# Optimization experiments

Hardware: AMD Instinct MI355X
Metric: run time of the kernel (lower is better)

The kernel has to match this reference:

```python
import jax, jax.numpy as jnp
import numpy as np

NEG_SLOPE = 0.2  # PyG GATv2Conv default negative_slope
HEADS = 4


def _gatv2_layer(x, src, dst, Wl, bl, Wr, br, att, bias):
    """GATv2Conv, concat=False (mean over heads), add_self_loops handled by caller.
    x: [N, Fin]; src/dst: [E] (message src -> dst); Wl/Wr: [Fin, H*C]; att: [H, C].
    """
    N = x.shape[0]
    H, C = att.shape
    xl = (x @ Wl + bl).reshape(N, H, C)  # source-side transform
    xr = (x @ Wr + br).reshape(N, H, C)  # target-side transform
    e = jax.nn.leaky_relu(xl[src] + xr[dst], NEG_SLOPE)          # [E, H, C]
    logits = jnp.einsum('ehc,hc->eh', e, att)                     # [E, H]
    # segment softmax over incoming edges of each target node
    m = jax.ops.segment_max(logits, dst, num_segments=N)          # [N, H]
    a = jnp.exp(logits - m[dst])
    denom = jax.ops.segment_sum(a, dst, num_segments=N)
    alpha = a / denom[dst]                                        # [E, H]
    out = jax.ops.segment_sum(alpha[:, :, None] * xl[src], dst, num_segments=N)  # [N, H, C]
    return out.mean(axis=1) + bias                                # concat=False -> head mean


def _glorot(k, shape):
    fan_in, fan_out = shape[0], shape[1] if len(shape) > 1 else shape[0]
    s = jnp.sqrt(2.0 / (fan_in + fan_out)).astype(jnp.float32)
    return jax.random.normal(k, shape, jnp.float32) * s


def setup_inputs() -> dict:
    key = jax.random.key(0)
    ks = jax.random.split(key, 24)
    N, E = 50000, 512000
    x = jax.random.normal(ks[0], (N, 9), jnp.float32)
    src = jax.random.randint(ks[1], (E,), 0, N, dtype=jnp.int32)
    dst = jax.random.randint(ks[2], (E,), 0, N, dtype=jnp.int32)
    dst = jnp.where(src == dst, (dst + 1) % N, dst)  # PyG removes self-loops then re-adds them
    edge_index = jnp.stack([src, dst])
    dims = [(9, 64), (64, 64), (64, 128)]  # (Fin, C_out) per layer
    inp = {'x': x, 'edge_index': edge_index}
    ki = 3
    for i, (fi, co) in enumerate(dims):
        inp[f'Wl{i}'] = _glorot(ks[ki], (fi, HEADS * co)); ki += 1
        inp[f'bl{i}'] = jnp.zeros((HEADS * co,), jnp.float32)
        inp[f'Wr{i}'] = _glorot(ks[ki], (fi, HEADS * co)); ki += 1
        inp[f'br{i}'] = jnp.zeros((HEADS * co,), jnp.float32)
        inp[f'att{i}'] = _glorot(ks[ki], (HEADS, co)); ki += 1
        inp[f'b{i}'] = jnp.zeros((co,), jnp.float32)
    return inp


def reference(x, edge_index, Wl0, bl0, Wr0, br0, att0, b0,
              Wl1, bl1, Wr1, br1, att1, b1,
              Wl2, bl2, Wr2, br2, att2, b2):
    N = x.shape[0]
    loops = jnp.arange(N, dtype=edge_index.dtype)
    src = jnp.concatenate([edge_index[0], loops])  # add self-loops (PyG default)
    dst = jnp.concatenate([edge_index[1], loops])
    h = _gatv2_layer(x, src, dst, Wl0, bl0, Wr0, br0, att0, b0)
    h = jax.nn.relu(h)  # dropout: eval mode -> identity
    h = _gatv2_layer(h, src, dst, Wl1, bl1, Wr1, br1, att1, b1)
    h = jax.nn.relu(h)
    out = _gatv2_layer(h, src, dst, Wl2, bl2, Wr2, br2, att2, b2)
    return out
```

## Files before the change

kernel.cpp:

```cpp
#include <hip/hip_runtime.h>
#include <hip/hip_bf16.h>


typedef __attribute__((ext_vector_type(8))) short bf16x8;
typedef __attribute__((ext_vector_type(4))) float f32x4;

__device__ __forceinline__ float bflo(unsigned w) { return __uint_as_float(w << 16); }
__device__ __forceinline__ float bfhi(unsigned w) { return __uint_as_float(w & 0xffff0000u); }
__device__ __forceinline__ unsigned short f2bf(float v) {
    unsigned u = __float_as_uint(v);
    u = (u + 0x7fff + ((u >> 16) & 1)) >> 16;
    return (unsigned short)u;
}
__device__ __forceinline__ float bf2f(unsigned short h) {
    return __uint_as_float((unsigned)h << 16);
}


__global__ void zero_int_k(int* p, int n) {
    int i = blockIdx.x * 256 + threadIdx.x;
    if (i < n) p[i] = 0;
}

__global__ void count_k(const int* __restrict__ dst, int* __restrict__ cnt,
                        int E, int EP) {
    int e = blockIdx.x * 256 + threadIdx.x;
    if (e >= EP) return;
    int d = (e < E) ? dst[e] : (e - E);
    atomicAdd(&cnt[d], 1);
}

__global__ void scan1_k(const int* __restrict__ cnt, int* __restrict__ offs,
                        int* __restrict__ partial, int N) {
    __shared__ int buf[2][1024];
    int g = blockIdx.x * 1024 + threadIdx.x;
    int v = (g < N) ? cnt[g] : 0;
    int pi = 0;
    buf[0][threadIdx.x] = v;
    __syncthreads();
    for (int s = 1; s < 1024; s <<= 1) {
        int t = buf[pi][threadIdx.x];
        if ((int)threadIdx.x >= s) t += buf[pi][threadIdx.x - s];
        buf[pi ^ 1][threadIdx.x] = t;
        pi ^= 1;
        __syncthreads();
    }
    int incl = buf[pi][threadIdx.x];
    if (g < N) offs[g + 1] = incl;
    if (threadIdx.x == 1023) partial[blockIdx.x] = incl;
}

__global__ void scan2_k(int* partial, int nb) {
    if (blockIdx.x == 0 && threadIdx.x == 0) {
        int run = 0;
        for (int i = 0; i < nb; i++) { int t = partial[i]; partial[i] = run; run += t; }
    }
}

__global__ void scan3_k(int* __restrict__ offs, const int* __restrict__ partial, int N) {
    int g = blockIdx.x * 1024 + threadIdx.x;
    if (g < N) offs[g + 1] += partial[blockIdx.x];
    if (g == 0) offs[0] = 0;
}

__global__ void fill2_k(const int* __restrict__ src, const int* __restrict__ dst,
                        const int* __restrict__ offs, int* __restrict__ cnt2,
                        int* __restrict__ csrc, int E, int EP) {
    int e = blockIdx.x * 256 + threadIdx.x;
    if (e >= EP) return;
    int sv, d;
    if (e < E) { sv = src[e]; d = dst[e]; }
    else       { sv = e - E;  d = sv; }
    int p = offs[d] + atomicAdd(&cnt2[d], 1);
    csrc[p] = sv;
}

template <int FIN>
__global__ void gemm2_bf16_k(const float* __restrict__ X,
                             const float* __restrict__ Wl, const float* __restrict__ bl,
                             const float* __restrict__ Wr, const float* __restrict__ br,
                             unsigned short* __restrict__ xl, unsigned short* __restrict__ xr,
                             int N, int HCT) {
    constexpr int RPT = 16;
    __shared__ float Xs[RPT][FIN];
    int tid  = threadIdx.x;
    int col  = blockIdx.y * 256 + tid;
    int row0 = blockIdx.x * RPT;
    for (int i = tid; i < RPT * FIN; i += 256) {
        int r = i / FIN, k = i % FIN;
        int gr = row0 + r;
        Xs[r][k] = (gr < N) ? X[(size_t)gr * FIN + k] : 0.f;
    }
    __syncthreads();
    float aL[RPT], aR[RPT];
    float b1 = bl[col], b2 = br[col];
#pragma unroll
    for (int r = 0; r < RPT; r++) { aL[r] = b1; aR[r] = b2; }
    for (int k = 0; k < FIN; k++) {
        float wl = Wl[(size_t)k * HCT + col];
        float wr = Wr[(size_t)k * HCT + col];
#pragma unroll
        for (int r = 0; r < RPT; r++) {
            float xv = Xs[r][k];
            aL[r] = fmaf(xv, wl, aL[r]);
            aR[r] = fmaf(xv, wr, aR[r]);
        }
    }
#pragma unroll
    for (int r = 0; r < RPT; r++) {
        int gr = row0 + r;
        if (gr < N) {
            xl[(size_t)gr * HCT + col] = f2bf(aL[r]);
            xr[(size_t)gr * HCT + col] = f2bf(aR[r]);
        }
    }
}

__device__ __forceinline__ void pack_one(const float* Wl, const float* Wr,
                                         unsigned short* Wh, unsigned short* Wlo,
                                         int HCT, int t) {
    int j  = t & 7;
    int l  = (t >> 3) & 63;
    int ks = (t >> 9) & 1;
    int ct = t >> 10;
    int k  = ks * 32 + (l >> 4) * 8 + j;
    int cg = ct * 16 + (l & 15);
    float v = (cg < HCT) ? Wl[(size_t)k * HCT + cg] : Wr[(size_t)k * HCT + (cg - HCT)];
    unsigned short hi = f2bf(v);
    Wh[t]  = hi;
    Wlo[t] = f2bf(v - bf2f(hi));
}

__global__ void split_w2_k(const float* __restrict__ Wl1, const float* __restrict__ Wr1,
                           unsigned short* __restrict__ W1h, unsigned short* __restrict__ W1l,
                           const float* __restrict__ Wl2, const float* __restrict__ Wr2,
                           unsigned short* __restrict__ W2h, unsigned short* __restrict__ W2l) {
    int tid = blockIdx.x * 256 + threadIdx.x;
    if (tid < 32 * 1024) pack_one(Wl1, Wr1, W1h, W1l, 256, tid);
    else                 pack_one(Wl2, Wr2, W2h, W2l, 512, tid - 32 * 1024);
}

template <int CHUNKS>
__global__ void mfma_gemm_k(const unsigned short* __restrict__ Ahi,
                            const unsigned short* __restrict__ Alo,
                            const unsigned short* __restrict__ Wphi,
                            const unsigned short* __restrict__ Wplo,
                            const float* __restrict__ bl, const float* __restrict__ br,
                            unsigned short* __restrict__ xl, unsigned short* __restrict__ xr,
                            int N, int HCT) {
    __shared__ float lds[4][16][128];
    int tid = threadIdx.x;
    int w   = tid >> 6, l = tid & 63;
    int l15 = l & 15,  seg = l >> 4;
    int row  = blockIdx.x * 64 + w * 16 + l15;
    int arow = (row < N) ? row : (N - 1);

    bf16x8 a0h = *(const bf16x8*)(Ahi + (size_t)arow * 64 + seg * 8);
    bf16x8 a1h = *(const bf16x8*)(Ahi + (size_t)arow * 64 + 32 + seg * 8);
    bf16x8 a0l = *(const bf16x8*)(Alo + (size_t)arow * 64 + seg * 8);
    bf16x8 a1l = *(const bf16x8*)(Alo + (size_t)arow * 64 + 32 + seg * 8);

    for (int c = 0; c < CHUNKS; c++) {
        int mat   = (c * 128) / HCT;
        int mcol0 = (c * 128) % HCT;
        const float* bias = mat ? br : bl;
        unsigned short* out = mat ? xr : xl;
        f32x4 acc[8];
#pragma unroll
        for (int t = 0; t < 8; t++) {
            float bv = bias[mcol0 + t * 16 + l15];
            acc[t] = (f32x4){bv, bv, bv, bv};
        }
#pragma unroll
        for (int t = 0; t < 8; t++) {
            size_t ct = (size_t)(c * 8 + t);
            bf16x8 b0h = *(const bf16x8*)(Wphi + ((ct * 2    ) * 64 + l) * 8);
            bf16x8 b1h = *(const bf16x8*)(Wphi + ((ct * 2 + 1) * 64 + l) * 8);
            bf16x8 b0l = *(const bf16x8*)(Wplo + ((ct * 2    ) * 64 + l) * 8);
            bf16x8 b1l = *(const bf16x8*)(Wplo + ((ct * 2 + 1) * 64 + l) * 8);
            acc[t] = __builtin_amdgcn_mfma_f32_16x16x32_bf16(a0h, b0h, acc[t], 0, 0, 0);
            acc[t] = __builtin_amdgcn_mfma_f32_16x16x32_bf16(a1h, b1h, acc[t], 0, 0, 0);
            acc[t] = __builtin_amdgcn_mfma_f32_16x16x32_bf16(a0l, b0h, acc[t], 0, 0, 0);
            acc[t] = __builtin_amdgcn_mfma_f32_16x16x32_bf16(a1l, b1h, acc[t], 0, 0, 0);
            acc[t] = __builtin_amdgcn_mfma_f32_16x16x32_bf16(a0h, b0l, acc[t], 0, 0, 0);
            acc[t] = __builtin_amdgcn_mfma_f32_16x16x32_bf16(a1h, b1l, acc[t], 0, 0, 0);
        }
#pragma unroll
        for (int t = 0; t < 8; t++)
#pragma unroll
            for (int r = 0; r < 4; r++)
                lds[w][seg * 4 + r][t * 16 + l15] = acc[t][r];
#pragma unroll
        for (int r = 0; r < 16; r++) {
            int orow = blockIdx.x * 64 + w * 16 + r;
            if (orow < N) {
                float v0 = lds[w][r][2 * l];
                float v1 = lds[w][r][2 * l + 1];
                unsigned pack = (unsigned)f2bf(v0) | ((unsigned)f2bf(v1) << 16);
                *(unsigned*)(out + (size_t)orow * HCT + mcol0 + 2 * l) = pack;
            }
        }
    }
}

template <int F, int OUT>
__global__ void node_fused_k(const unsigned short* __restrict__ xl,
                             const unsigned short* __restrict__ xr,
                             const float* __restrict__ att, const float* __restrict__ bias,
                             const int* __restrict__ offs, const int* __restrict__ csrc,
                             unsigned short* __restrict__ Yhi, unsigned short* __restrict__ Ylo,
                             float* __restrict__ out, int N) {
    constexpr int HCT = 64 * F;
    constexpr int NW  = F / 2;
    int wv   = blockIdx.x * 4 + (threadIdx.x >> 6);
    int lane = threadIdx.x & 63;
    if (wv >= N) return;

    float xrv[F], at[F];
    {
        const unsigned* xp = (const unsigned*)(xr + (size_t)wv * HCT + lane * F);
#pragma unroll
        for (int i = 0; i < NW; i++) {
            unsigned w = xp[i];
            xrv[2 * i] = bflo(w); xrv[2 * i + 1] = bfhi(w);
        }
#pragma unroll
        for (int i = 0; i < F; i++) at[i] = att[lane * F + i];
    }

    int o0 = offs[wv], o1 = offs[wv + 1];
    float m = -1e30f, s = 0.f;
    float acc[F];
#pragma unroll
    for (int i = 0; i < F; i++) acc[i] = 0.f;

    for (int j = o0; j < o1; ++j) {
        int sn = csrc[j];
        const unsigned* xp = (const unsigned*)(xl + (size_t)sn * HCT + lane * F);
        float xv[F];
#pragma unroll
        for (int i = 0; i < NW; i++) {
            unsigned w = xp[i];
            xv[2 * i] = bflo(w); xv[2 * i + 1] = bfhi(w);
        }
        float p1 = 0.f, p2 = 0.f;
#pragma unroll
        for (int i = 0; i < F; i++) {
            float a = xv[i] + xrv[i];
            p1 = fmaf(at[i], a, p1);
            p2 = fmaf(at[i], fabsf(a), p2);
        }
        float p = fmaf(0.6f, p1, 0.4f * p2);
        p += __shfl_xor(p, 1, 64);
        p += __shfl_xor(p, 2, 64);
        p += __shfl_xor(p, 4, 64);
        p += __shfl_xor(p, 8, 64);
        if (__any(p > m + 20.f)) {
            float nm = fmaxf(m, p);
            float r  = __expf(m - nm);
            float w  = __expf(p - nm);
            s = fmaf(s, r, w);
#pragma unroll
            for (int i = 0; i < F; i++) acc[i] = fmaf(acc[i], r, w * xv[i]);
            m = nm;
        } else {
            float w = __expf(p - m);
            s += w;
#pragma unroll
            for (int i = 0; i < F; i++) acc[i] = fmaf(w, xv[i], acc[i]);
        }
    }

    float inv = 1.f / s;
#pragma unroll
    for (int i = 0; i < F; i++) acc[i] *= inv;
#pragma unroll
    for (int i = 0; i < F; i++) {
        acc[i] += __shfl_xor(acc[i], 16, 64);
        acc[i] += __shfl_xor(acc[i], 32, 64);
    }
    if (lane < 16) {
        if (OUT == 0) {
            unsigned short h[F], lo[F];
#pragma unroll
            for (int i = 0; i < F; i++) {
                float v = fmaf(acc[i], 0.25f, bias[lane * F + i]);
                v = fmaxf(v, 0.f);
                h[i] = f2bf(v);
                lo[i] = f2bf(v - bf2f(h[i]));
            }
            size_t base = (size_t)wv * (16 * F) + lane * F;
#pragma unroll
            for (int i = 0; i < F / 2; i++) {
                ((unsigned*)(Yhi + base))[i] = (unsigned)h[2 * i] | ((unsigned)h[2 * i + 1] << 16);
                ((unsigned*)(Ylo + base))[i] = (unsigned)lo[2 * i] | ((unsigned)lo[2 * i + 1] << 16);
            }
        } else {
            float* op = out + (size_t)wv * (16 * F) + lane * F;
#pragma unroll
            for (int i = 0; i < F; i++)
                op[i] = fmaf(acc[i], 0.25f, bias[lane * F + i]);
        }
    }
}


static inline size_t align256(size_t x) { return (x + 255) & ~(size_t)255; }

extern "C" void kernel_launch(void* const* d_in, const int* in_sizes, int n_in,
                              void* d_out, int out_size, void* d_ws, size_t ws_size,
                              hipStream_t stream) {
    const float* x  = (const float*)d_in[0];
    const int*   ei = (const int*)d_in[1];
    const int N  = in_sizes[0] / 9;
    const int E  = in_sizes[1] / 2;
    const int EP = E + N;
    const int* src = ei;
    const int* dst = ei + E;

    const float *Wl[3], *bl[3], *Wr[3], *br[3], *att[3], *bb[3];
    for (int i = 0; i < 3; i++) {
        Wl[i]  = (const float*)d_in[2 + 6 * i];
        bl[i]  = (const float*)d_in[3 + 6 * i];
        Wr[i]  = (const float*)d_in[4 + 6 * i];
        br[i]  = (const float*)d_in[5 + 6 * i];
        att[i] = (const float*)d_in[6 + 6 * i];
        bb[i]  = (const float*)d_in[7 + 6 * i];
    }

    char* w = (char*)d_ws;
    unsigned short* xl  = (unsigned short*)w; w += align256((size_t)N * 512 * 2);
    unsigned short* xr  = (unsigned short*)w; w += align256((size_t)N * 512 * 2);
    unsigned short* A1h = (unsigned short*)w; w += align256((size_t)N * 64 * 2);
    unsigned short* A1l = (unsigned short*)w; w += align256((size_t)N * 64 * 2);
    unsigned short* A2h = (unsigned short*)w; w += align256((size_t)N * 64 * 2);
    unsigned short* A2l = (unsigned short*)w; w += align256((size_t)N * 64 * 2);
    int* offs   = (int*)w;  w += align256((size_t)(N + 1) * 4);
    int* cnt    = (int*)w;  w += align256((size_t)(2 * N) * 4);
    int* csrc   = (int*)w;  w += align256((size_t)EP * 4);
    int* partial = (int*)w; w += 4096;
    unsigned short* Wp1h = (unsigned short*)w; w += align256((size_t)32 * 1024 * 2);
    unsigned short* Wp1l = (unsigned short*)w; w += align256((size_t)32 * 1024 * 2);
    unsigned short* Wp2h = (unsigned short*)w; w += align256((size_t)64 * 1024 * 2);
    unsigned short* Wp2l = (unsigned short*)w; w += align256((size_t)64 * 1024 * 2);
    int* cnt2 = cnt + N;

    zero_int_k<<<(2 * N + 255) / 256, 256, 0, stream>>>(cnt, 2 * N);
    count_k<<<(EP + 255) / 256, 256, 0, stream>>>(dst, cnt, E, EP);
    int nb = (N + 1023) / 1024;
    scan1_k<<<nb, 1024, 0, stream>>>(cnt, offs, partial, N);
    scan2_k<<<1, 64, 0, stream>>>(partial, nb);
    scan3_k<<<nb, 1024, 0, stream>>>(offs, partial, N);
    fill2_k<<<(EP + 255) / 256, 256, 0, stream>>>(src, dst, offs, cnt2, csrc, E, EP);

    split_w2_k<<<(96 * 1024) / 256, 256, 0, stream>>>(
        Wl[1], Wr[1], Wp1h, Wp1l, Wl[2], Wr[2], Wp2h, Wp2l);

    const int nodeBlocks = (N + 3) / 4;
    const int gemmBlocks = (N + 63) / 64;

    dim3 g1((N + 15) / 16, 1);
    gemm2_bf16_k<9><<<g1, 256, 0, stream>>>(
        x, Wl[0], bl[0], Wr[0], br[0], xl, xr, N, 256);
    node_fused_k<4, 0><<<nodeBlocks, 256, 0, stream>>>(
        xl, xr, att[0], bb[0], offs, csrc, A1h, A1l, nullptr, N);

    mfma_gemm_k<4><<<gemmBlocks, 256, 0, stream>>>(
        A1h, A1l, Wp1h, Wp1l, bl[1], br[1], xl, xr, N, 256);
    node_fused_k<4, 0><<<nodeBlocks, 256, 0, stream>>>(
        xl, xr, att[1], bb[1], offs, csrc, A2h, A2l, nullptr, N);

    mfma_gemm_k<8><<<gemmBlocks, 256, 0, stream>>>(
        A2h, A2l, Wp2h, Wp2l, bl[2], br[2], xl, xr, N, 512);
    node_fused_k<8, 1><<<nodeBlocks, 256, 0, stream>>>(
        xl, xr, att[2], bb[2], offs, csrc, nullptr, nullptr, (float*)d_out, N);
}
```

Before: 463.3 us.

## Store xl/xr in fp16, use packed fdot2 for attention logits, merge scan passes

The projected features xl/xr are now stored as fp16 instead of bf16. The edge loop adds them with packed half arithmetic and computes the attention dot products with fdot2 intrinsics. The aggregation accumulates a+xl (already summed) and subtracts xr once at the end, which reuses the sum instead of reconverting xl. The two scan fixup kernels are merged into one that computes block prefixes with a wave reduction. The intent is to cut ALU work in the gather-bound node kernel. It risks fp16 overflow or precision loss, and the end-of-loop subtraction assumes the softmax weights sum to one.

```diff
diff --git a/kernel.cpp b/kernel.cpp
--- a/kernel.cpp
+++ b/kernel.cpp
@@ -4,9 +4,10 @@
 
 typedef __attribute__((ext_vector_type(8))) short bf16x8;
 typedef __attribute__((ext_vector_type(4))) float f32x4;
-
-__device__ __forceinline__ float bflo(unsigned w) { return __uint_as_float(w << 16); }
-__device__ __forceinline__ float bfhi(unsigned w) { return __uint_as_float(w & 0xffff0000u); }
+typedef _Float16 f16;
+typedef __attribute__((ext_vector_type(2))) _Float16 h2;
+typedef __attribute__((ext_vector_type(2))) float f2;
+
 __device__ __forceinline__ unsigned short f2bf(float v) {
     unsigned u = __float_as_uint(v);
     u = (u + 0x7fff + ((u >> 16) & 1)) >> 16;
@@ -50,17 +51,23 @@
     if (threadIdx.x == 1023) partial[blockIdx.x] = incl;
 }
 
-__global__ void scan2_k(int* partial, int nb) {
-    if (blockIdx.x == 0 && threadIdx.x == 0) {
-        int run = 0;
-        for (int i = 0; i < nb; i++) { int t = partial[i]; partial[i] = run; run += t; }
-    }
-}
-
-__global__ void scan3_k(int* __restrict__ offs, const int* __restrict__ partial, int N) {
-    int g = blockIdx.x * 1024 + threadIdx.x;
-    if (g < N) offs[g + 1] += partial[blockIdx.x];
+__global__ void scan23_k(int* __restrict__ offs, const int* __restrict__ partial, int N) {
+    __shared__ float dummy;
+    __shared__ int preS;
+    int b = blockIdx.x;
+    if (threadIdx.x < 64) {
+        int t = threadIdx.x;
+        int v = (t < b) ? partial[t] : 0;
+#pragma unroll
+        for (int o = 32; o > 0; o >>= 1) v += __shfl_xor(v, o, 64);
+        if (t == 0) preS = v;
+    }
+    __syncthreads();
+    int pre = preS;
+    int g = b * 1024 + threadIdx.x;
+    if (g < N) offs[g + 1] += pre;
     if (g == 0) offs[0] = 0;
+    (void)dummy;
 }
 
 __global__ void fill2_k(const int* __restrict__ src, const int* __restrict__ dst,
@@ -76,11 +83,11 @@
 }
 
 template <int FIN>
-__global__ void gemm2_bf16_k(const float* __restrict__ X,
-                             const float* __restrict__ Wl, const float* __restrict__ bl,
-                             const float* __restrict__ Wr, const float* __restrict__ br,
-                             unsigned short* __restrict__ xl, unsigned short* __restrict__ xr,
-                             int N, int HCT) {
+__global__ void gemm2_f16_k(const float* __restrict__ X,
+                            const float* __restrict__ Wl, const float* __restrict__ bl,
+                            const float* __restrict__ Wr, const float* __restrict__ br,
+                            unsigned short* __restrict__ xl, unsigned short* __restrict__ xr,
+                            int N, int HCT) {
     constexpr int RPT = 16;
     __shared__ float Xs[RPT][FIN];
     int tid  = threadIdx.x;
@@ -110,8 +117,8 @@
     for (int r = 0; r < RPT; r++) {
         int gr = row0 + r;
         if (gr < N) {
-            xl[(size_t)gr * HCT + col] = f2bf(aL[r]);
-            xr[(size_t)gr * HCT + col] = f2bf(aR[r]);
+            xl[(size_t)gr * HCT + col] = __builtin_bit_cast(unsigned short, (f16)aL[r]);
+            xr[(size_t)gr * HCT + col] = __builtin_bit_cast(unsigned short, (f16)aR[r]);
         }
     }
 }
@@ -196,8 +203,9 @@
             if (orow < N) {
                 float v0 = lds[w][r][2 * l];
                 float v1 = lds[w][r][2 * l + 1];
-                unsigned pack = (unsigned)f2bf(v0) | ((unsigned)f2bf(v1) << 16);
-                *(unsigned*)(out + (size_t)orow * HCT + mcol0 + 2 * l) = pack;
+                h2 hv = { (f16)v0, (f16)v1 };
+                *(unsigned*)(out + (size_t)orow * HCT + mcol0 + 2 * l) =
+                    __builtin_bit_cast(unsigned, hv);
             }
         }
     }
@@ -216,75 +224,85 @@
     int lane = threadIdx.x & 63;
     if (wv >= N) return;
 
-    float xrv[F], at[F];
+    h2 xrh[NW], ath[NW];
+    f2 xrf[NW];
     {
         const unsigned* xp = (const unsigned*)(xr + (size_t)wv * HCT + lane * F);
 #pragma unroll
         for (int i = 0; i < NW; i++) {
-            unsigned w = xp[i];
-            xrv[2 * i] = bflo(w); xrv[2 * i + 1] = bfhi(w);
-        }
-#pragma unroll
-        for (int i = 0; i < F; i++) at[i] = att[lane * F + i];
+            xrh[i] = __builtin_bit_cast(h2, xp[i]);
+            xrf[i] = __builtin_convertvector(xrh[i], f2);
+            ath[i] = h2{ (f16)att[lane * F + 2 * i], (f16)att[lane * F + 2 * i + 1] };
+        }
     }
 
     int o0 = offs[wv], o1 = offs[wv + 1];
     float m = -1e30f, s = 0.f;
-    float acc[F];
-#pragma unroll
-    for (int i = 0; i < F; i++) acc[i] = 0.f;
+    f2 acc[NW];
+#pragma unroll
+    for (int i = 0; i < NW; i++) acc[i] = f2{0.f, 0.f};
 
     for (int j = o0; j < o1; ++j) {
         int sn = csrc[j];
         const unsigned* xp = (const unsigned*)(xl + (size_t)sn * HCT + lane * F);
-        float xv[F];
+        h2 a[NW];
+        float p1 = 0.f, p2 = 0.f;
 #pragma unroll
         for (int i = 0; i < NW; i++) {
-            unsigned w = xp[i];
-            xv[2 * i] = bflo(w); xv[2 * i + 1] = bfhi(w);
-        }
-        float p1 = 0.f, p2 = 0.f;
-#pragma unroll
-        for (int i = 0; i < F; i++) {
-            float a = xv[i] + xrv[i];
-            p1 = fmaf(at[i], a, p1);
-            p2 = fmaf(at[i], fabsf(a), p2);
+            h2 xv = __builtin_bit_cast(h2, xp[i]);
+            a[i] = xv + xrh[i];
+            unsigned au = __builtin_bit_cast(unsigned, a[i]) & 0x7FFF7FFFu;
+            h2 aa = __builtin_bit_cast(h2, au);
+            p1 = __builtin_amdgcn_fdot2(ath[i], a[i], p1, false);
+            p2 = __builtin_amdgcn_fdot2(ath[i], aa,   p2, false);
         }
         float p = fmaf(0.6f, p1, 0.4f * p2);
         p += __shfl_xor(p, 1, 64);
         p += __shfl_xor(p, 2, 64);
         p += __shfl_xor(p, 4, 64);
         p += __shfl_xor(p, 8, 64);
+        f2 af[NW];
+#pragma unroll
+        for (int i = 0; i < NW; i++) af[i] = __builtin_convertvector(a[i], f2);
         if (__any(p > m + 20.f)) {
             float nm = fmaxf(m, p);
             float r  = __expf(m - nm);
             float w  = __expf(p - nm);
             s = fmaf(s, r, w);
-#pragma unroll
-            for (int i = 0; i < F; i++) acc[i] = fmaf(acc[i], r, w * xv[i]);
+            f2 r2 = {r, r}, w2 = {w, w};
+#pragma unroll
+            for (int i = 0; i < NW; i++)
+                acc[i] = __builtin_elementwise_fma(acc[i], r2, af[i] * w2);
             m = nm;
         } else {
             float w = __expf(p - m);
             s += w;
-#pragma unroll
-            for (int i = 0; i < F; i++) acc[i] = fmaf(w, xv[i], acc[i]);
+            f2 w2 = {w, w};
+#pragma unroll
+            for (int i = 0; i < NW; i++)
+                acc[i] = __builtin_elementwise_fma(af[i], w2, acc[i]);
         }
     }
 
     float inv = 1.f / s;
-#pragma unroll
-    for (int i = 0; i < F; i++) acc[i] *= inv;
+    f2 inv2 = {inv, inv};
+    float val[F];
+#pragma unroll
+    for (int i = 0; i < NW; i++) {
+        f2 v = __builtin_elementwise_fma(acc[i], inv2, -xrf[i]);
+        val[2 * i] = v.x; val[2 * i + 1] = v.y;
+    }
 #pragma unroll
     for (int i = 0; i < F; i++) {
-        acc[i] += __shfl_xor(acc[i], 16, 64);
-        acc[i] += __shfl_xor(acc[i], 32, 64);
+        val[i] += __shfl_xor(val[i], 16, 64);
+        val[i] += __shfl_xor(val[i], 32, 64);
     }
     if (lane < 16) {
         if (OUT == 0) {
             unsigned short h[F], lo[F];
 #pragma unroll
             for (int i = 0; i < F; i++) {
-                float v = fmaf(acc[i], 0.25f, bias[lane * F + i]);
+                float v = fmaf(val[i], 0.25f, bias[lane * F + i]);
                 v = fmaxf(v, 0.f);
                 h[i] = f2bf(v);
                 lo[i] = f2bf(v - bf2f(h[i]));
@@ -299,7 +317,7 @@
             float* op = out + (size_t)wv * (16 * F) + lane * F;
 #pragma unroll
             for (int i = 0; i < F; i++)
-                op[i] = fmaf(acc[i], 0.25f, bias[lane * F + i]);
+                op[i] = fmaf(val[i], 0.25f, bias[lane * F + i]);
         }
     }
 }
@@ -349,8 +367,7 @@
     count_k<<<(EP + 255) / 256, 256, 0, stream>>>(dst, cnt, E, EP);
     int nb = (N + 1023) / 1024;
     scan1_k<<<nb, 1024, 0, stream>>>(cnt, offs, partial, N);
-    scan2_k<<<1, 64, 0, stream>>>(partial, nb);
-    scan3_k<<<nb, 1024, 0, stream>>>(offs, partial, N);
+    scan23_k<<<nb, 1024, 0, stream>>>(offs, partial, N);
     fill2_k<<<(EP + 255) / 256, 256, 0, stream>>>(src, dst, offs, cnt2, csrc, E, EP);
 
     split_w2_k<<<(96 * 1024) / 256, 256, 0, stream>>>(
@@ -360,7 +377,7 @@
     const int gemmBlocks = (N + 63) / 64;
 
     dim3 g1((N + 15) / 16, 1);
-    gemm2_bf16_k<9><<<g1, 256, 0, stream>>>(
+    gemm2_f16_k<9><<<g1, 256, 0, stream>>>(
         x, Wl[0], bl[0], Wr[0], br[0], xl, xr, N, 256);
     node_fused_k<4, 0><<<nodeBlocks, 256, 0, stream>>>(
         xl, xr, att[0], bb[0], offs, csrc, A1h, A1l, nullptr, N);
```

After: 455.4 us. About the same (-1.7%).
